# Kernel optimization log

Hardware: AMD Instinct MI355X
Metric: run time of the kernel (lower is better)

## Reference

```python
import jax, jax.numpy as jnp
import numpy as np

F, H1, H2, K, L = 16, 64, 64, 8, 8          # n_features, hidden sizes, num_bins, num_layers
NBP = 3 * K + 1                              # num_bijector_params per feature
RMIN, RMAX = -10.0, 10.0
MIN_BIN, MIN_SLOPE = 1e-4, 1e-4              # distrax RationalQuadraticSpline defaults


def setup_inputs() -> dict:
    key = jax.random.key(0)
    ks = jax.random.split(key, 11)
    B = 131072
    return {
        "x": jax.random.normal(ks[0], (B, F), jnp.float32),
        "W0": jax.random.normal(ks[1], (L, F, F), jnp.float32) * 0.1,
        "b0": jax.random.normal(ks[2], (L, F), jnp.float32) * 0.01,
        "W1": jax.random.normal(ks[3], (L, F, H1), jnp.float32) * 0.1,
        "b1": jax.random.normal(ks[4], (L, H1), jnp.float32) * 0.01,
        "W2": jax.random.normal(ks[5], (L, H1, H2), jnp.float32) * 0.1,
        "b2": jax.random.normal(ks[6], (L, H2), jnp.float32) * 0.01,
        "Wout": jax.random.normal(ks[7], (L, H2, F * NBP), jnp.float32) * 0.05,
        "bout": jax.random.normal(ks[8], (L, F * NBP), jnp.float32) * 0.01,
        # scalar-affine coupling params; scale kept positive (init is ones in the module)
        "scale": jnp.exp(0.05 * jax.random.normal(ks[9], (L, F), jnp.float32)),
        "shift": jax.random.normal(ks[10], (L, F), jnp.float32) * 0.1,
    }


def _rq_spline_fwd(params, x):
    """distrax.RationalQuadraticSpline forward_and_log_det (elementwise).
    params: (B, F, 3K+1), x: (B, F) -> (y, log_det) each (B, F)."""
    uw, uh, ud = params[..., :K], params[..., K:2 * K], params[..., 2 * K:]
    total = RMAX - RMIN
    w = jax.nn.softmax(uw, axis=-1) * (total - K * MIN_BIN) + MIN_BIN   # bin widths
    h = jax.nn.softmax(uh, axis=-1) * (total - K * MIN_BIN) + MIN_BIN   # bin heights
    offset = float(np.log(np.expm1(1.0 - MIN_SLOPE)))                   # softplus(0+offset)=1
    d = jax.nn.softplus(ud + offset) + MIN_SLOPE                        # knot slopes (B,F,K+1)
    zeros = jnp.zeros(w.shape[:-1] + (1,), w.dtype)
    xpos = RMIN + jnp.concatenate([zeros, jnp.cumsum(w, -1)], -1)       # knot x (B,F,K+1)
    ypos = RMIN + jnp.concatenate([zeros, jnp.cumsum(h, -1)], -1)       # knot y (B,F,K+1)
    # per-element bin search
    idx = jnp.clip(jnp.sum((x[..., None] >= xpos).astype(jnp.int32), -1) - 1, 0, K - 1)
    take = lambda a: jnp.take_along_axis(a, idx[..., None], axis=-1)[..., 0]
    xk, xk1 = take(xpos[..., :-1]), take(xpos[..., 1:])
    yk, yk1 = take(ypos[..., :-1]), take(ypos[..., 1:])
    dk, dk1 = take(d[..., :-1]), take(d[..., 1:])
    bw = xk1 - xk
    bh = yk1 - yk
    s = bh / bw                                                          # bin slope
    z = jnp.clip((x - xk) / bw, 0.0, 1.0)
    z1m = 1.0 - z
    den = s + (dk1 + dk - 2.0 * s) * z * z1m
    y = yk + bh * (s * z * z + dk * z * z1m) / den
    num_ld = dk1 * z * z + 2.0 * s * z * z1m + dk * z1m * z1m
    ld = 2.0 * jnp.log(s) + jnp.log(num_ld) - 2.0 * jnp.log(den)
    outside = (x <= RMIN) | (x >= RMAX)                                  # identity outside range
    return jnp.where(outside, x, y), jnp.where(outside, 0.0, ld)


def reference(x, W0, b0, W1, b1, W2, b2, Wout, bout, scale, shift):
    """log_prob of Transformed(base, Inverse(Chain(layers))) == base.log_prob(Chain.fwd(x)) + fwd logdet."""
    B = x.shape[0]
    feat = jnp.arange(F)
    z = x
    logdet = jnp.zeros((B,), x.dtype)
    # distrax.Chain applies the last-appended layer first -> iterate layers in reverse;
    # within layer i: spline coupling (appended second) then scalar-affine coupling.
    for i in reversed(range(L)):
        mask = ((feat + i) % 2).astype(bool)        # True = pass-through / conditioner input
        mz = jnp.where(mask, z, 0.0)
        hid = jnp.tanh(mz @ W0[i] + b0[i])
        hid = jnp.tanh(hid @ W1[i] + b1[i])
        hid = hid @ W2[i] + b2[i]                   # last MLP layer is linear
        p = (hid @ Wout[i] + bout[i]).reshape(B, F, NBP)
        y, ld = _rq_spline_fwd(p, z)
        z = jnp.where(mask, z, y)
        logdet = logdet + jnp.sum(jnp.where(mask, 0.0, ld), axis=-1)
        # scalar affine coupling with all-False mask: transforms every feature
        z = z * scale[i] + shift[i]
        logdet = logdet + jnp.sum(jnp.log(jnp.abs(scale[i])))
    base_lp = -0.5 * jnp.sum(z * z, axis=-1) - 0.5 * F * float(np.log(2.0 * np.pi))
    return base_lp + logdet
```

## Files before the change

kernel.cpp:

```cpp
#include <hip/hip_runtime.h>
#include <math.h>

typedef _Float16 f16;
typedef _Float16 half8 __attribute__((ext_vector_type(8)));
typedef float f32x16 __attribute__((ext_vector_type(16)));

#define DEV __device__ __forceinline__

#define W1F_OFF 0
#define W2F_OFF 16384
#define WOF_OFF 81920
#define BOF_OFF 344064
#define SUMLOG_OFF 352256

#define H0_OFF    0
#define H0_STRIDE 48
#define H_OFF     12288
#define H_STRIDE  144
#define P_OFF     49152
#define P_STRIDE  116
#define LDS_BYTES 78848

DEV float frcp(float x){ return __builtin_amdgcn_rcpf(x); }
DEV float fexp(float x){ return __expf(x); }
DEV float flog(float x){ return __logf(x); }

DEV float ftanh(float x){
  float e = fexp(2.f * x);
  float r = frcp(e + 1.f);
  return fmaf(-2.f, r, 1.f);
}

DEV void rq_spline(const float p[25], float xv, float &y_out, float &ld_out)
{
  float ew[8]; float sw = 0.f;
#pragma unroll
  for (int k = 0; k < 8; ++k){ ew[k] = fexp(p[k]); sw += ew[k]; }
  float rw = frcp(sw) * 19.9992f;

  float xpos[9];
  xpos[0] = -10.f;
#pragma unroll
  for (int k = 0; k < 8; ++k) xpos[k + 1] = xpos[k] + fmaf(ew[k], rw, 1e-4f);

  int idx = 0;
#pragma unroll
  for (int j = 1; j < 8; ++j) idx += (xv >= xpos[j]) ? 1 : 0;

  float xk = xpos[0], ewk = ew[0];
#pragma unroll
  for (int j = 1; j < 8; ++j){
    bool sel = (idx >= j);
    xk  = sel ? xpos[j] : xk;
    ewk = sel ? ew[j]   : ewk;
  }
  float bw = fmaf(ewk, rw, 1e-4f);

  float eh[8]; float shs = 0.f;
#pragma unroll
  for (int k = 0; k < 8; ++k){ eh[k] = fexp(p[8 + k]); shs += eh[k]; }
  float rh = frcp(shs) * 19.9992f;

  float S = 0.f, ehk = eh[0];
#pragma unroll
  for (int k = 1; k < 8; ++k){
    bool sel = (idx >= k);
    S   += sel ? eh[k - 1] : 0.f;
    ehk  = sel ? eh[k]     : ehk;
  }
  float yk = fmaf(S, rh, fmaf((float)idx, 1e-4f, -10.f));
  float bh = fmaf(ehk, rh, 1e-4f);

  float uA = p[16], uB = p[17];
#pragma unroll
  for (int j = 1; j < 8; ++j){
    bool sel = (idx >= j);
    uA = sel ? p[16 + j] : uA;
    uB = sel ? p[17 + j] : uB;
  }
  float vA = uA + 0.54116666f;
  float dk  = fmaxf(vA, 0.f) + flog(1.f + fexp(-fabsf(vA))) + 1e-4f;
  float vB = uB + 0.54116666f;
  float dk1 = fmaxf(vB, 0.f) + flog(1.f + fexp(-fabsf(vB))) + 1e-4f;

  float rbw = frcp(bw);
  float s   = bh * rbw;
  float zf  = fminf(fmaxf((xv - xk) * rbw, 0.f), 1.f);
  float z1  = 1.f - zf;
  float zz  = zf * zf, z01 = zf * z1;
  float den = s + (dk1 + dk - 2.f * s) * z01;
  float rden = frcp(den);
  float yv  = yk + bh * (s * zz + dk * z01) * rden;
  float num = dk1 * zz + 2.f * s * z01 + dk * z1 * z1;
  float ldv = flog(s * s * num * rden * rden);

  bool outside = (xv <= -10.f) || (xv >= 10.f);
  y_out  = outside ? xv : yv;
  ld_out = outside ? 0.f : ldv;
}

extern "C" __global__ void __launch_bounds__(256)
prep_kernel(const float* __restrict__ W1, const float* __restrict__ W2,
            const float* __restrict__ Wo, const float* __restrict__ bout,
            const float* __restrict__ scale, char* __restrict__ ws)
{
  int tid = blockIdx.x * 256 + threadIdx.x;
  if (tid < 1024){
    int fi = tid >> 6, lane = tid & 63;
    int l = fi >> 1, nt = fi & 1;
    int n = nt * 32 + (lane & 31), khi = lane >> 5;
    half8 h;
#pragma unroll
    for (int j = 0; j < 8; ++j){ int k = khi * 8 + j; h[j] = (f16)W1[l * 1024 + k * 64 + n]; }
    *(half8*)(ws + W1F_OFF + fi * 1024 + lane * 16) = h;
  } else if (tid < 5120){
    int idx = tid - 1024;
    int fi = idx >> 6, lane = idx & 63;
    int l = fi >> 3, kt = (fi >> 1) & 3, nt = fi & 1;
    int n = nt * 32 + (lane & 31), khi = lane >> 5;
    half8 h;
#pragma unroll
    for (int j = 0; j < 8; ++j){ int k = kt * 16 + khi * 8 + j; h[j] = (f16)W2[l * 4096 + k * 64 + n]; }
    *(half8*)(ws + W2F_OFF + fi * 1024 + lane * 16) = h;
  } else if (tid < 21504){
    int idx = tid - 5120;
    int fi = idx >> 6, lane = idx & 63;
    int l = fi >> 5, u = (fi >> 2) & 7, kt = fi & 3;
    int f = (l & 1) + 2 * u;
    int c = lane & 31, khi = lane >> 5;
    half8 h;
#pragma unroll
    for (int j = 0; j < 8; ++j){
      int k = kt * 16 + khi * 8 + j;
      float v = (c < 25) ? Wo[l * 25600 + k * 400 + f * 25 + c] : 0.f;
      h[j] = (f16)v;
    }
    *(half8*)(ws + WOF_OFF + fi * 1024 + lane * 16) = h;
  } else if (tid < 23552){
    int idx = tid - 21504;
    int l = idx >> 8, u = (idx >> 5) & 7, c = idx & 31;
    int f = (l & 1) + 2 * u;
    float v = (c < 25) ? bout[l * 400 + f * 25 + c] : 0.f;
    ((float*)(ws + BOF_OFF))[idx] = v;
  } else if (tid == 23552){
    float acc = 0.f;
    for (int i = 0; i < 128; ++i) acc += logf(fabsf(scale[i]));
    *(float*)(ws + SUMLOG_OFF) = acc;
  }
}

template<int PAR>
DEV void layer_mfma(int l,
                    const float* __restrict__ W0, const float* __restrict__ b0,
                    const float* __restrict__ b1v, const float* __restrict__ b2v,
                    const float* __restrict__ scv, const float* __restrict__ shv,
                    const char* __restrict__ ws, char* lds,
                    float (&z)[16], float &logdet,
                    int t, int lane, int wv, int ln31, int khi)
{
  const float* w0  = W0 + l * 256;
  const float* bb0 = b0 + l * 16;
  const int rowbase = khi * 4;

  const half8* W1F = (const half8*)(ws + W1F_OFF);
  const half8* W2F = (const half8*)(ws + W2F_OFF);
  half8 w1f[2];
#pragma unroll
  for (int nt = 0; nt < 2; ++nt) w1f[nt] = W1F[(l * 2 + nt) * 64 + lane];
  half8 w2f[8];
#pragma unroll
  for (int kt = 0; kt < 4; ++kt)
#pragma unroll
    for (int nt = 0; nt < 2; ++nt)
      w2f[kt * 2 + nt] = W2F[((l * 4 + kt) * 2 + nt) * 64 + lane];
  float bias1[2], bias2[2];
#pragma unroll
  for (int nt = 0; nt < 2; ++nt){
    bias1[nt] = b1v[l * 64 + nt * 32 + ln31];
    bias2[nt] = b2v[l * 64 + nt * 32 + ln31];
  }

  float h0[16];
#pragma unroll
  for (int j = 0; j < 16; ++j) h0[j] = bb0[j];
#pragma unroll
  for (int u = 0; u < 8; ++u){
    const int f = (1 - PAR) + 2 * u;
    const float v = z[f];
#pragma unroll
    for (int j = 0; j < 16; ++j) h0[j] = fmaf(v, w0[f * 16 + j], h0[j]);
  }
  {
    half8 lo, hi;
#pragma unroll
    for (int j = 0; j < 8; ++j){ lo[j] = (f16)ftanh(h0[j]); hi[j] = (f16)ftanh(h0[8 + j]); }
    *(half8*)(lds + H0_OFF + t * H0_STRIDE)      = lo;
    *(half8*)(lds + H0_OFF + t * H0_STRIDE + 16) = hi;
  }

  half8 a0[2];
#pragma unroll
  for (int mt = 0; mt < 2; ++mt){
    int s = wv * 64 + mt * 32 + ln31;
    a0[mt] = *(const half8*)(lds + H0_OFF + s * H0_STRIDE + khi * 16);
  }
  f32x16 d1[2][2];
#pragma unroll
  for (int mt = 0; mt < 2; ++mt)
#pragma unroll
    for (int nt = 0; nt < 2; ++nt)
#pragma unroll
      for (int i = 0; i < 16; ++i) d1[mt][nt][i] = bias1[nt];
#pragma unroll
  for (int nt = 0; nt < 2; ++nt)
#pragma unroll
    for (int mt = 0; mt < 2; ++mt)
      d1[mt][nt] = __builtin_amdgcn_mfma_f32_32x32x16_f16(a0[mt], w1f[nt], d1[mt][nt], 0, 0, 0);
#pragma unroll
  for (int mt = 0; mt < 2; ++mt)
#pragma unroll
    for (int nt = 0; nt < 2; ++nt)
#pragma unroll
      for (int i = 0; i < 16; ++i){
        int row = (i & 3) + 8 * (i >> 2) + rowbase;
        int s = wv * 64 + mt * 32 + row;
        float v = ftanh(d1[mt][nt][i]);
        *(f16*)(lds + H_OFF + s * H_STRIDE + (nt * 32 + ln31) * 2) = (f16)v;
      }

  half8 a1[2][4];
#pragma unroll
  for (int mt = 0; mt < 2; ++mt){
    int s = wv * 64 + mt * 32 + ln31;
#pragma unroll
    for (int kt = 0; kt < 4; ++kt)
      a1[mt][kt] = *(const half8*)(lds + H_OFF + s * H_STRIDE + kt * 32 + khi * 16);
  }
  f32x16 d2[2][2];
#pragma unroll
  for (int mt = 0; mt < 2; ++mt)
#pragma unroll
    for (int nt = 0; nt < 2; ++nt)
#pragma unroll
      for (int i = 0; i < 16; ++i) d2[mt][nt][i] = bias2[nt];
#pragma unroll
  for (int kt = 0; kt < 4; ++kt)
#pragma unroll
    for (int nt = 0; nt < 2; ++nt)
#pragma unroll
      for (int mt = 0; mt < 2; ++mt)
        d2[mt][nt] = __builtin_amdgcn_mfma_f32_32x32x16_f16(a1[mt][kt], w2f[kt * 2 + nt], d2[mt][nt], 0, 0, 0);

  const half8* WOF = (const half8*)(ws + WOF_OFF);
  const float* BOF = (const float*)(ws + BOF_OFF);
  half8 bfn[4];
#pragma unroll
  for (int kt = 0; kt < 4; ++kt) bfn[kt] = WOF[((l * 8 + 0) * 4 + kt) * 64 + lane];
  float biasn = BOF[(l * 8 + 0) * 32 + ln31];

#pragma unroll
  for (int mt = 0; mt < 2; ++mt)
#pragma unroll
    for (int nt = 0; nt < 2; ++nt)
#pragma unroll
      for (int i = 0; i < 16; ++i){
        int row = (i & 3) + 8 * (i >> 2) + rowbase;
        int s = wv * 64 + mt * 32 + row;
        float v = d2[mt][nt][i];
        *(f16*)(lds + H_OFF + s * H_STRIDE + (nt * 32 + ln31) * 2) = (f16)v;
      }

  half8 a2[2][4];
#pragma unroll
  for (int mt = 0; mt < 2; ++mt){
    int s = wv * 64 + mt * 32 + ln31;
#pragma unroll
    for (int kt = 0; kt < 4; ++kt)
      a2[mt][kt] = *(const half8*)(lds + H_OFF + s * H_STRIDE + kt * 32 + khi * 16);
  }

  {
    f32x16 dp[2];
#pragma unroll
    for (int mt = 0; mt < 2; ++mt)
#pragma unroll
      for (int i = 0; i < 16; ++i) dp[mt][i] = biasn;
#pragma unroll
    for (int kt = 0; kt < 4; ++kt)
#pragma unroll
      for (int mt = 0; mt < 2; ++mt)
        dp[mt] = __builtin_amdgcn_mfma_f32_32x32x16_f16(a2[mt][kt], bfn[kt], dp[mt], 0, 0, 0);
    if (ln31 < 25){
#pragma unroll
      for (int mt = 0; mt < 2; ++mt)
#pragma unroll
        for (int i = 0; i < 16; ++i){
          int row = (i & 3) + 8 * (i >> 2) + rowbase;
          int s = wv * 64 + mt * 32 + row;
          *(float*)(lds + P_OFF + s * P_STRIDE + ln31 * 4) = dp[mt][i];
        }
    }
  }
#pragma unroll
  for (int kt = 0; kt < 4; ++kt) bfn[kt] = WOF[((l * 8 + 1) * 4 + kt) * 64 + lane];
  biasn = BOF[(l * 8 + 1) * 32 + ln31];

#pragma unroll 1
  for (int u = 0; u < 8; ++u){
    float p[25];
#pragma unroll
    for (int j = 0; j < 25; ++j)
      p[j] = *(const float*)(lds + P_OFF + t * P_STRIDE + j * 4);

    if (u < 7){
      f32x16 dp[2];
#pragma unroll
      for (int mt = 0; mt < 2; ++mt)
#pragma unroll
        for (int i = 0; i < 16; ++i) dp[mt][i] = biasn;
#pragma unroll
      for (int kt = 0; kt < 4; ++kt)
#pragma unroll
        for (int mt = 0; mt < 2; ++mt)
          dp[mt] = __builtin_amdgcn_mfma_f32_32x32x16_f16(a2[mt][kt], bfn[kt], dp[mt], 0, 0, 0);
      if (ln31 < 25){
#pragma unroll
        for (int mt = 0; mt < 2; ++mt)
#pragma unroll
          for (int i = 0; i < 16; ++i){
            int row = (i & 3) + 8 * (i >> 2) + rowbase;
            int s = wv * 64 + mt * 32 + row;
            *(float*)(lds + P_OFF + s * P_STRIDE + ln31 * 4) = dp[mt][i];
          }
      }
      if (u < 6){
#pragma unroll
        for (int kt = 0; kt < 4; ++kt) bfn[kt] = WOF[((l * 8 + u + 2) * 4 + kt) * 64 + lane];
        biasn = BOF[(l * 8 + u + 2) * 32 + ln31];
      }
    }

    const int f = PAR + 2 * u;
    float y, ld;
    rq_spline(p, z[f], y, ld);
    z[f] = y;
    logdet += ld;
  }

  const float* scp = scv + l * 16;
  const float* shp = shv + l * 16;
#pragma unroll
  for (int j = 0; j < 16; ++j)
    z[j] = fmaf(z[j], scp[j], shp[j]);
}

extern "C" __global__ void __launch_bounds__(256, 2)
flow_kernel(const float* __restrict__ x,
            const float* __restrict__ W0, const float* __restrict__ b0,
            const float* __restrict__ b1v, const float* __restrict__ b2v,
            const float* __restrict__ scv, const float* __restrict__ shv,
            const char* __restrict__ ws, float* __restrict__ out, int B)
{
  extern __shared__ char lds[];
  const int t    = threadIdx.x;
  const int lane = t & 63;
  const int wv   = t >> 6;
  const int ln31 = lane & 31;
  const int khi  = lane >> 5;
  const int g    = blockIdx.x * 256 + t;

  float z[16];
  const float4* xv = reinterpret_cast<const float4*>(x + (size_t)g * 16);
  float4 a0 = xv[0], a1 = xv[1], a2 = xv[2], a3 = xv[3];
  z[0]=a0.x; z[1]=a0.y; z[2]=a0.z; z[3]=a0.w;
  z[4]=a1.x; z[5]=a1.y; z[6]=a1.z; z[7]=a1.w;
  z[8]=a2.x; z[9]=a2.y; z[10]=a2.z; z[11]=a2.w;
  z[12]=a3.x; z[13]=a3.y; z[14]=a3.z; z[15]=a3.w;

  float logdet = 0.f;
  for (int l = 7; l >= 0; --l){
    if (l & 1) layer_mfma<1>(l, W0, b0, b1v, b2v, scv, shv, ws, lds, z, logdet, t, lane, wv, ln31, khi);
    else       layer_mfma<0>(l, W0, b0, b1v, b2v, scv, shv, ws, lds, z, logdet, t, lane, wv, ln31, khi);
  }

  float sumlog = *(const float*)(ws + SUMLOG_OFF);
  float ss = 0.f;
#pragma unroll
  for (int j = 0; j < 16; ++j) ss = fmaf(z[j], z[j], ss);
  out[g] = -0.5f * ss - 14.7030165f + logdet + sumlog;
}

extern "C" void kernel_launch(void* const* d_in, const int* in_sizes, int n_in,
                              void* d_out, int out_size, void* d_ws, size_t ws_size,
                              hipStream_t stream)
{
  const float* x    = (const float*)d_in[0];
  const float* W0   = (const float*)d_in[1];
  const float* b0   = (const float*)d_in[2];
  const float* W1   = (const float*)d_in[3];
  const float* b1   = (const float*)d_in[4];
  const float* W2   = (const float*)d_in[5];
  const float* b2   = (const float*)d_in[6];
  const float* Wout = (const float*)d_in[7];
  const float* bout = (const float*)d_in[8];
  const float* scale= (const float*)d_in[9];
  const float* shift= (const float*)d_in[10];

  int B = in_sizes[0] / 16;

  hipLaunchKernelGGL(prep_kernel, dim3(93), dim3(256), 0, stream,
                     W1, W2, Wout, bout, scale, (char*)d_ws);

  hipLaunchKernelGGL(flow_kernel, dim3(B / 256), dim3(256), LDS_BYTES, stream,
                     x, W0, b0, b1, b2, scale, shift,
                     (const char*)d_ws, (float*)d_out, B);
}
```

Measured before the change: 209.2 us.

## Map 32 samples per wave with lane halves splitting spline features

```diff
diff --git a/kernel.cpp b/kernel.cpp
--- a/kernel.cpp
+++ b/kernel.cpp
@@ -13,13 +13,11 @@
 #define BOF_OFF 344064
 #define SUMLOG_OFF 352256
 
-#define H0_OFF    0
-#define H0_STRIDE 48
-#define H_OFF     12288
 #define H_STRIDE  144
-#define P_OFF     49152
 #define P_STRIDE  116
-#define LDS_BYTES 78848
+#define P_SLOT    3712
+#define ARENA     7424
+#define LDS_BYTES (4 * ARENA)
 
 DEV float frcp(float x){ return __builtin_amdgcn_rcpf(x); }
 DEV float fexp(float x){ return __expf(x); }
@@ -43,16 +41,16 @@
 #pragma unroll
   for (int k = 0; k < 8; ++k) xpos[k + 1] = xpos[k] + fmaf(ew[k], rw, 1e-4f);
 
+  bool b[8];
   int idx = 0;
 #pragma unroll
-  for (int j = 1; j < 8; ++j) idx += (xv >= xpos[j]) ? 1 : 0;
+  for (int j = 1; j < 8; ++j){ b[j] = (xv >= xpos[j]); idx += b[j] ? 1 : 0; }
 
   float xk = xpos[0], ewk = ew[0];
 #pragma unroll
   for (int j = 1; j < 8; ++j){
-    bool sel = (idx >= j);
-    xk  = sel ? xpos[j] : xk;
-    ewk = sel ? ew[j]   : ewk;
+    xk  = b[j] ? xpos[j] : xk;
+    ewk = b[j] ? ew[j]   : ewk;
   }
   float bw = fmaf(ewk, rw, 1e-4f);
 
@@ -64,9 +62,8 @@
   float S = 0.f, ehk = eh[0];
 #pragma unroll
   for (int k = 1; k < 8; ++k){
-    bool sel = (idx >= k);
-    S   += sel ? eh[k - 1] : 0.f;
-    ehk  = sel ? eh[k]     : ehk;
+    S   += b[k] ? eh[k - 1] : 0.f;
+    ehk  = b[k] ? eh[k]     : ehk;
   }
   float yk = fmaf(S, rh, fmaf((float)idx, 1e-4f, -10.f));
   float bh = fmaf(ehk, rh, 1e-4f);
@@ -74,9 +71,8 @@
   float uA = p[16], uB = p[17];
 #pragma unroll
   for (int j = 1; j < 8; ++j){
-    bool sel = (idx >= j);
-    uA = sel ? p[16 + j] : uA;
-    uB = sel ? p[17 + j] : uB;
+    uA = b[j] ? p[16 + j] : uA;
+    uB = b[j] ? p[17 + j] : uB;
   }
   float vA = uA + 0.54116666f;
   float dk  = fmaxf(vA, 0.f) + flog(1.f + fexp(-fabsf(vA))) + 1e-4f;
@@ -156,7 +152,7 @@
                     const float* __restrict__ scv, const float* __restrict__ shv,
                     const char* __restrict__ ws, char* lds,
                     float (&z)[16], float &logdet,
-                    int t, int lane, int wv, int ln31, int khi)
+                    int lane, int ln31, int khi)
 {
   const float* w0  = W0 + l * 256;
   const float* bb0 = b0 + l * 16;
@@ -180,170 +176,144 @@
     bias2[nt] = b2v[l * 64 + nt * 32 + ln31];
   }
 
-  float h0[16];
-#pragma unroll
-  for (int j = 0; j < 16; ++j) h0[j] = bb0[j];
+  const int j0 = khi * 8;
+  float h0[8];
+#pragma unroll
+  for (int j = 0; j < 8; ++j) h0[j] = bb0[j0 + j];
 #pragma unroll
   for (int u = 0; u < 8; ++u){
     const int f = (1 - PAR) + 2 * u;
     const float v = z[f];
 #pragma unroll
-    for (int j = 0; j < 16; ++j) h0[j] = fmaf(v, w0[f * 16 + j], h0[j]);
-  }
-  {
-    half8 lo, hi;
-#pragma unroll
-    for (int j = 0; j < 8; ++j){ lo[j] = (f16)ftanh(h0[j]); hi[j] = (f16)ftanh(h0[8 + j]); }
-    *(half8*)(lds + H0_OFF + t * H0_STRIDE)      = lo;
-    *(half8*)(lds + H0_OFF + t * H0_STRIDE + 16) = hi;
-  }
-
-  half8 a0[2];
-#pragma unroll
-  for (int mt = 0; mt < 2; ++mt){
-    int s = wv * 64 + mt * 32 + ln31;
-    a0[mt] = *(const half8*)(lds + H0_OFF + s * H0_STRIDE + khi * 16);
-  }
-  f32x16 d1[2][2];
-#pragma unroll
-  for (int mt = 0; mt < 2; ++mt)
+    for (int j = 0; j < 8; ++j) h0[j] = fmaf(v, w0[f * 16 + j0 + j], h0[j]);
+  }
+  half8 a0;
+#pragma unroll
+  for (int j = 0; j < 8; ++j) a0[j] = (f16)ftanh(h0[j]);
+
+  f32x16 d1[2];
+#pragma unroll
+  for (int nt = 0; nt < 2; ++nt)
+#pragma unroll
+    for (int i = 0; i < 16; ++i) d1[nt][i] = bias1[nt];
+#pragma unroll
+  for (int nt = 0; nt < 2; ++nt)
+    d1[nt] = __builtin_amdgcn_mfma_f32_32x32x16_f16(a0, w1f[nt], d1[nt], 0, 0, 0);
+#pragma unroll
+  for (int nt = 0; nt < 2; ++nt)
+#pragma unroll
+    for (int i = 0; i < 16; ++i){
+      int row = (i & 3) + 8 * (i >> 2) + rowbase;
+      float v = ftanh(d1[nt][i]);
+      *(f16*)(lds + row * H_STRIDE + (nt * 32 + ln31) * 2) = (f16)v;
+    }
+
+  half8 a1[4];
+#pragma unroll
+  for (int kt = 0; kt < 4; ++kt)
+    a1[kt] = *(const half8*)(lds + ln31 * H_STRIDE + kt * 32 + khi * 16);
+  f32x16 d2[2];
+#pragma unroll
+  for (int nt = 0; nt < 2; ++nt)
+#pragma unroll
+    for (int i = 0; i < 16; ++i) d2[nt][i] = bias2[nt];
+#pragma unroll
+  for (int kt = 0; kt < 4; ++kt)
 #pragma unroll
     for (int nt = 0; nt < 2; ++nt)
-#pragma unroll
-      for (int i = 0; i < 16; ++i) d1[mt][nt][i] = bias1[nt];
-#pragma unroll
-  for (int nt = 0; nt < 2; ++nt)
-#pragma unroll
-    for (int mt = 0; mt < 2; ++mt)
-      d1[mt][nt] = __builtin_amdgcn_mfma_f32_32x32x16_f16(a0[mt], w1f[nt], d1[mt][nt], 0, 0, 0);
-#pragma unroll
-  for (int mt = 0; mt < 2; ++mt)
-#pragma unroll
-    for (int nt = 0; nt < 2; ++nt)
+      d2[nt] = __builtin_amdgcn_mfma_f32_32x32x16_f16(a1[kt], w2f[kt * 2 + nt], d2[nt], 0, 0, 0);
+
+  const half8* WOF = (const half8*)(ws + WOF_OFF);
+  const float* BOF = (const float*)(ws + BOF_OFF);
+  half8 bfn[2][4]; float biasn[2];
+#pragma unroll
+  for (int h = 0; h < 2; ++h){
+    const int u = h * 4;
+#pragma unroll
+    for (int kt = 0; kt < 4; ++kt) bfn[h][kt] = WOF[((l * 8 + u) * 4 + kt) * 64 + lane];
+    biasn[h] = BOF[(l * 8 + u) * 32 + ln31];
+  }
+
+#pragma unroll
+  for (int nt = 0; nt < 2; ++nt)
+#pragma unroll
+    for (int i = 0; i < 16; ++i){
+      int row = (i & 3) + 8 * (i >> 2) + rowbase;
+      *(f16*)(lds + row * H_STRIDE + (nt * 32 + ln31) * 2) = (f16)d2[nt][i];
+    }
+
+  half8 a2[4];
+#pragma unroll
+  for (int kt = 0; kt < 4; ++kt)
+    a2[kt] = *(const half8*)(lds + ln31 * H_STRIDE + kt * 32 + khi * 16);
+
+#pragma unroll
+  for (int h = 0; h < 2; ++h){
+    f32x16 dp;
+#pragma unroll
+    for (int i = 0; i < 16; ++i) dp[i] = biasn[h];
+#pragma unroll
+    for (int kt = 0; kt < 4; ++kt)
+      dp = __builtin_amdgcn_mfma_f32_32x32x16_f16(a2[kt], bfn[h][kt], dp, 0, 0, 0);
+    if (ln31 < 25){
 #pragma unroll
       for (int i = 0; i < 16; ++i){
         int row = (i & 3) + 8 * (i >> 2) + rowbase;
-        int s = wv * 64 + mt * 32 + row;
-        float v = ftanh(d1[mt][nt][i]);
-        *(f16*)(lds + H_OFF + s * H_STRIDE + (nt * 32 + ln31) * 2) = (f16)v;
+        *(float*)(lds + h * P_SLOT + row * P_STRIDE + ln31 * 4) = dp[i];
       }
-
-  half8 a1[2][4];
-#pragma unroll
-  for (int mt = 0; mt < 2; ++mt){
-    int s = wv * 64 + mt * 32 + ln31;
-#pragma unroll
-    for (int kt = 0; kt < 4; ++kt)
-      a1[mt][kt] = *(const half8*)(lds + H_OFF + s * H_STRIDE + kt * 32 + khi * 16);
-  }
-  f32x16 d2[2][2];
-#pragma unroll
-  for (int mt = 0; mt < 2; ++mt)
-#pragma unroll
-    for (int nt = 0; nt < 2; ++nt)
-#pragma unroll
-      for (int i = 0; i < 16; ++i) d2[mt][nt][i] = bias2[nt];
-#pragma unroll
-  for (int kt = 0; kt < 4; ++kt)
-#pragma unroll
-    for (int nt = 0; nt < 2; ++nt)
-#pragma unroll
-      for (int mt = 0; mt < 2; ++mt)
-        d2[mt][nt] = __builtin_amdgcn_mfma_f32_32x32x16_f16(a1[mt][kt], w2f[kt * 2 + nt], d2[mt][nt], 0, 0, 0);
-
-  const half8* WOF = (const half8*)(ws + WOF_OFF);
-  const float* BOF = (const float*)(ws + BOF_OFF);
-  half8 bfn[4];
-#pragma unroll
-  for (int kt = 0; kt < 4; ++kt) bfn[kt] = WOF[((l * 8 + 0) * 4 + kt) * 64 + lane];
-  float biasn = BOF[(l * 8 + 0) * 32 + ln31];
-
-#pragma unroll
-  for (int mt = 0; mt < 2; ++mt)
-#pragma unroll
-    for (int nt = 0; nt < 2; ++nt)
-#pragma unroll
-      for (int i = 0; i < 16; ++i){
-        int row = (i & 3) + 8 * (i >> 2) + rowbase;
-        int s = wv * 64 + mt * 32 + row;
-        float v = d2[mt][nt][i];
-        *(f16*)(lds + H_OFF + s * H_STRIDE + (nt * 32 + ln31) * 2) = (f16)v;
-      }
-
-  half8 a2[2][4];
-#pragma unroll
-  for (int mt = 0; mt < 2; ++mt){
-    int s = wv * 64 + mt * 32 + ln31;
-#pragma unroll
-    for (int kt = 0; kt < 4; ++kt)
-      a2[mt][kt] = *(const half8*)(lds + H_OFF + s * H_STRIDE + kt * 32 + khi * 16);
-  }
-
-  {
-    f32x16 dp[2];
-#pragma unroll
-    for (int mt = 0; mt < 2; ++mt)
-#pragma unroll
-      for (int i = 0; i < 16; ++i) dp[mt][i] = biasn;
-#pragma unroll
-    for (int kt = 0; kt < 4; ++kt)
-#pragma unroll
-      for (int mt = 0; mt < 2; ++mt)
-        dp[mt] = __builtin_amdgcn_mfma_f32_32x32x16_f16(a2[mt][kt], bfn[kt], dp[mt], 0, 0, 0);
-    if (ln31 < 25){
-#pragma unroll
-      for (int mt = 0; mt < 2; ++mt)
-#pragma unroll
-        for (int i = 0; i < 16; ++i){
-          int row = (i & 3) + 8 * (i >> 2) + rowbase;
-          int s = wv * 64 + mt * 32 + row;
-          *(float*)(lds + P_OFF + s * P_STRIDE + ln31 * 4) = dp[mt][i];
-        }
-    }
-  }
-#pragma unroll
-  for (int kt = 0; kt < 4; ++kt) bfn[kt] = WOF[((l * 8 + 1) * 4 + kt) * 64 + lane];
-  biasn = BOF[(l * 8 + 1) * 32 + ln31];
+    }
+  }
+#pragma unroll
+  for (int h = 0; h < 2; ++h){
+    const int u = h * 4 + 1;
+#pragma unroll
+    for (int kt = 0; kt < 4; ++kt) bfn[h][kt] = WOF[((l * 8 + u) * 4 + kt) * 64 + lane];
+    biasn[h] = BOF[(l * 8 + u) * 32 + ln31];
+  }
 
 #pragma unroll 1
-  for (int u = 0; u < 8; ++u){
+  for (int v = 0; v < 4; ++v){
     float p[25];
 #pragma unroll
     for (int j = 0; j < 25; ++j)
-      p[j] = *(const float*)(lds + P_OFF + t * P_STRIDE + j * 4);
-
-    if (u < 7){
-      f32x16 dp[2];
-#pragma unroll
-      for (int mt = 0; mt < 2; ++mt)
-#pragma unroll
-        for (int i = 0; i < 16; ++i) dp[mt][i] = biasn;
-#pragma unroll
-      for (int kt = 0; kt < 4; ++kt)
-#pragma unroll
-        for (int mt = 0; mt < 2; ++mt)
-          dp[mt] = __builtin_amdgcn_mfma_f32_32x32x16_f16(a2[mt][kt], bfn[kt], dp[mt], 0, 0, 0);
-      if (ln31 < 25){
-#pragma unroll
-        for (int mt = 0; mt < 2; ++mt)
+      p[j] = *(const float*)(lds + khi * P_SLOT + ln31 * P_STRIDE + j * 4);
+
+    if (v < 3){
+#pragma unroll
+      for (int h = 0; h < 2; ++h){
+        f32x16 dp;
+#pragma unroll
+        for (int i = 0; i < 16; ++i) dp[i] = biasn[h];
+#pragma unroll
+        for (int kt = 0; kt < 4; ++kt)
+          dp = __builtin_amdgcn_mfma_f32_32x32x16_f16(a2[kt], bfn[h][kt], dp, 0, 0, 0);
+        if (ln31 < 25){
 #pragma unroll
           for (int i = 0; i < 16; ++i){
             int row = (i & 3) + 8 * (i >> 2) + rowbase;
-            int s = wv * 64 + mt * 32 + row;
-            *(float*)(lds + P_OFF + s * P_STRIDE + ln31 * 4) = dp[mt][i];
+            *(float*)(lds + h * P_SLOT + row * P_STRIDE + ln31 * 4) = dp[i];
           }
+        }
       }
-      if (u < 6){
-#pragma unroll
-        for (int kt = 0; kt < 4; ++kt) bfn[kt] = WOF[((l * 8 + u + 2) * 4 + kt) * 64 + lane];
-        biasn = BOF[(l * 8 + u + 2) * 32 + ln31];
+      if (v < 2){
+#pragma unroll
+        for (int h = 0; h < 2; ++h){
+          const int u = h * 4 + v + 2;
+#pragma unroll
+          for (int kt = 0; kt < 4; ++kt) bfn[h][kt] = WOF[((l * 8 + u) * 4 + kt) * 64 + lane];
+          biasn[h] = BOF[(l * 8 + u) * 32 + ln31];
+        }
       }
     }
 
-    const int f = PAR + 2 * u;
+    const int f0 = PAR + 2 * v;
+    const int f1 = f0 + 8;
+    float xv = khi ? z[f1] : z[f0];
     float y, ld;
-    rq_spline(p, z[f], y, ld);
-    z[f] = y;
+    rq_spline(p, xv, y, ld);
+    float yx = __shfl_xor(y, 32, 64);
+    z[f0] = khi ? yx : y;
+    z[f1] = khi ? y  : yx;
     logdet += ld;
   }
 
@@ -354,24 +324,25 @@
     z[j] = fmaf(z[j], scp[j], shp[j]);
 }
 
-extern "C" __global__ void __launch_bounds__(256, 2)
+extern "C" __global__ void __launch_bounds__(256, 4)
 flow_kernel(const float* __restrict__ x,
             const float* __restrict__ W0, const float* __restrict__ b0,
             const float* __restrict__ b1v, const float* __restrict__ b2v,
             const float* __restrict__ scv, const float* __restrict__ shv,
             const char* __restrict__ ws, float* __restrict__ out, int B)
 {
-  extern __shared__ char lds[];
+  extern __shared__ char lds_raw[];
   const int t    = threadIdx.x;
   const int lane = t & 63;
   const int wv   = t >> 6;
   const int ln31 = lane & 31;
   const int khi  = lane >> 5;
-  const int g    = blockIdx.x * 256 + t;
+  char* lds = lds_raw + wv * ARENA;
+  const int g = blockIdx.x * 128 + wv * 32 + ln31;
 
   float z[16];
-  const float4* xv = reinterpret_cast<const float4*>(x + (size_t)g * 16);
-  float4 a0 = xv[0], a1 = xv[1], a2 = xv[2], a3 = xv[3];
+  const float4* xv4 = reinterpret_cast<const float4*>(x + (size_t)g * 16);
+  float4 a0 = xv4[0], a1 = xv4[1], a2 = xv4[2], a3 = xv4[3];
   z[0]=a0.x; z[1]=a0.y; z[2]=a0.z; z[3]=a0.w;
   z[4]=a1.x; z[5]=a1.y; z[6]=a1.z; z[7]=a1.w;
   z[8]=a2.x; z[9]=a2.y; z[10]=a2.z; z[11]=a2.w;
@@ -379,15 +350,18 @@
 
   float logdet = 0.f;
   for (int l = 7; l >= 0; --l){
-    if (l & 1) layer_mfma<1>(l, W0, b0, b1v, b2v, scv, shv, ws, lds, z, logdet, t, lane, wv, ln31, khi);
-    else       layer_mfma<0>(l, W0, b0, b1v, b2v, scv, shv, ws, lds, z, logdet, t, lane, wv, ln31, khi);
-  }
+    if (l & 1) layer_mfma<1>(l, W0, b0, b1v, b2v, scv, shv, ws, lds, z, logdet, lane, ln31, khi);
+    else       layer_mfma<0>(l, W0, b0, b1v, b2v, scv, shv, ws, lds, z, logdet, lane, ln31, khi);
+  }
+
+  logdet += __shfl_xor(logdet, 32, 64);
 
   float sumlog = *(const float*)(ws + SUMLOG_OFF);
   float ss = 0.f;
 #pragma unroll
   for (int j = 0; j < 16; ++j) ss = fmaf(z[j], z[j], ss);
-  out[g] = -0.5f * ss - 14.7030165f + logdet + sumlog;
+  if (khi == 0)
+    out[g] = -0.5f * ss - 14.7030165f + logdet + sumlog;
 }
 
 extern "C" void kernel_launch(void* const* d_in, const int* in_sizes, int n_in,
@@ -411,7 +385,7 @@
   hipLaunchKernelGGL(prep_kernel, dim3(93), dim3(256), 0, stream,
                      W1, W2, Wout, bout, scale, (char*)d_ws);
 
-  hipLaunchKernelGGL(flow_kernel, dim3(B / 256), dim3(256), LDS_BYTES, stream,
+  hipLaunchKernelGGL(flow_kernel, dim3(B / 128), dim3(256), LDS_BYTES, stream,
                      x, W0, b0, b1, b2, scale, shift,
                      (const char*)d_ws, (float*)d_out, B);
 }
```

Result: slower. 377.7 us (+80.5%).
